# Performance work log

Hardware: AMD Instinct MI355X
Metric: run time of the kernel (lower is better)

The kernel has to match this reference:

```python
import jax, jax.numpy as jnp
import numpy as np

B, N, DIM, H, DH = 2, 2048, 1024, 16, 64
SOFTCAP = 50.0
SCALE = DH ** -0.5
EPS = 1e-12


def _rmsnorm(x, gamma):
    # F.normalize (l2norm over last dim) * sqrt(dim) * (gamma + 1)
    norm = jnp.maximum(jnp.linalg.norm(x, axis=-1, keepdims=True), EPS)
    return (x / norm) * (DIM ** 0.5) * (gamma + 1.0)


def _rotate_half(t):
    # interleaved pairs: (x1, x2) -> (-x2, x1), as in rotary_embedding_torch
    t = t.reshape(*t.shape[:-1], -1, 2)
    x1, x2 = t[..., 0], t[..., 1]
    return jnp.stack((-x2, x1), axis=-1).reshape(*t.shape[:-2], -1)


def _apply_rotary(freqs, t):
    # freqs: [n, d] broadcast over [b, h, n, d]
    return t * jnp.cos(freqs) + _rotate_half(t) * jnp.sin(freqs)


def setup_inputs() -> dict:
    key = jax.random.key(0)
    k0, k1, k2, k3, k4 = jax.random.split(key, 5)
    x = jax.random.normal(k0, (B, N, DIM), jnp.float32)
    gamma = jax.random.normal(k1, (DIM,), jnp.float32) * 0.02
    w_qkv = jax.random.normal(k2, (DIM, 3 * H * DH), jnp.float32) * 0.02
    w_out = jax.random.normal(k3, (H * DH, DIM), jnp.float32) * 0.02
    rotary_emb = jax.random.normal(k4, (N, DH), jnp.float32)
    attn_mask = jnp.broadcast_to(jnp.tril(jnp.ones((N, N), bool)), (B, N, N))
    return {"x": x, "attn_mask": attn_mask, "rotary_emb": rotary_emb,
            "gamma": gamma, "w_qkv": w_qkv, "w_out": w_out}


def reference(x, attn_mask, rotary_emb, gamma, w_qkv, w_out):
    x = _rmsnorm(x, gamma)
    qkv = (x @ w_qkv).reshape(B, N, 3, H, DH)        # b n (qkv h d)
    qkv = jnp.transpose(qkv, (2, 0, 3, 1, 4))        # qkv b h n d
    q, k, v = qkv[0], qkv[1], qkv[2]
    q = _apply_rotary(rotary_emb, q)
    k = _apply_rotary(rotary_emb, k)
    q = q * SCALE
    sim = jnp.einsum('bhid,bhjd->bhij', q, k)
    sim = jnp.tanh(sim / SOFTCAP) * SOFTCAP          # softclamp
    mask_value = -jnp.finfo(sim.dtype).max
    sim = jnp.where(attn_mask[:, None, :, :], sim, mask_value)
    attn = jax.nn.softmax(sim, axis=-1)
    out = jnp.einsum('bhij,bhjd->bhid', attn, v)
    out = jnp.transpose(out, (0, 2, 1, 3)).reshape(B, N, H * DH)  # b n (h d)
    return out @ w_out
```

## Files before the change

### kernel.cpp

```cpp
#include <hip/hip_runtime.h>
#include <hip/hip_bf16.h>

typedef unsigned short u16;
typedef unsigned int u32;
typedef __bf16 bf16x8 __attribute__((ext_vector_type(8)));
typedef float f32x4 __attribute__((ext_vector_type(4)));

#define NB 2
#define NSEQ 2048
#define NDIM 1024
#define NH 16
#define NDH 64

static __device__ __forceinline__ u16 f2bf(float f) {
  return __builtin_bit_cast(u16, (__bf16)f);
}
static __device__ __forceinline__ float bf2f(u16 u) {
  union { u32 u; float f; } a; a.u = ((u32)u) << 16; return a.f;
}
static __device__ __forceinline__ bf16x8 ldbf8(const u16* p) {
  return *(const bf16x8*)p;
}
static __device__ __forceinline__ f32x4 mfma16(bf16x8 a, bf16x8 b, f32x4 c) {
  return __builtin_amdgcn_mfma_f32_16x16x32_bf16(a, b, c, 0, 0, 0);
}
static __device__ __forceinline__ float fexp2(float x) {
  return __builtin_amdgcn_exp2f(x);
}
#define GLDS(g, d) __builtin_amdgcn_global_load_lds(                         \
    (const __attribute__((address_space(1))) void*)(g),                      \
    (__attribute__((address_space(3))) void*)(d), 16, 0, 0)

__global__ __launch_bounds__(256) void k_transpose(const float* __restrict__ in,
                                                   u16* __restrict__ out,
                                                   int R, int C) {
  __shared__ u16 tile[64][65];
  const int r0 = blockIdx.x * 64, c0 = blockIdx.y * 64;
  const int t = threadIdx.x;
  const int tr = t >> 6;
  const int tc = t & 63;
#pragma unroll 4
  for (int p = 0; p < 16; p++) {
    int r = p * 4 + tr;
    tile[r][tc] = f2bf(in[(size_t)(r0 + r) * C + (c0 + tc)]);
  }
  __syncthreads();
#pragma unroll 4
  for (int p = 0; p < 16; p++) {
    int rr = p * 4 + tr;
    out[(size_t)(c0 + rr) * R + (r0 + tc)] = tile[tc][rr];
  }
}

__global__ __launch_bounds__(256) void k_rmsnorm(const float* __restrict__ x,
                                                 const float* __restrict__ gamma,
                                                 u16* __restrict__ xn) {
  __shared__ float part[4];
  const int row = blockIdx.x;
  const int t = threadIdx.x;
  const float4 v = ((const float4*)(x + (size_t)row * NDIM))[t];
  float ss = v.x * v.x + v.y * v.y + v.z * v.z + v.w * v.w;
#pragma unroll
  for (int off = 1; off < 64; off <<= 1) ss += __shfl_xor(ss, off, 64);
  if ((t & 63) == 0) part[t >> 6] = ss;
  __syncthreads();
  const float tot = part[0] + part[1] + part[2] + part[3];
  const float scale = 32.0f / fmaxf(sqrtf(tot), 1e-12f);
  const float4 g = ((const float4*)gamma)[t];
  u16 o0 = f2bf(v.x * scale * (g.x + 1.0f));
  u16 o1 = f2bf(v.y * scale * (g.y + 1.0f));
  u16 o2 = f2bf(v.z * scale * (g.z + 1.0f));
  u16 o3 = f2bf(v.w * scale * (g.w + 1.0f));
  uint2 pv;
  pv.x = (u32)o0 | ((u32)o1 << 16);
  pv.y = (u32)o2 | ((u32)o3 << 16);
  *(uint2*)(xn + (size_t)row * NDIM + t * 4) = pv;
}

template <int EPI>
__global__ __launch_bounds__(256) void k_gemm_bt(const u16* __restrict__ A,
                                                 const u16* __restrict__ BT,
                                                 float* __restrict__ Of,
                                                 u16* __restrict__ O0,
                                                 u16* __restrict__ O1,
                                                 u16* __restrict__ O2) {
  constexpr int KD = 1024, BK = 64, NT = KD / BK;
  __shared__ u16 As[128 * BK];
  __shared__ u16 Bs[128 * BK];
  const int m0 = blockIdx.x * 128, n0 = blockIdx.y * 128;
  const int t = threadIdx.x;
  const int w = t >> 6, l = t & 63, lo = l & 15, hi = l >> 4;
  const int wr = (w >> 1) * 64, wc = (w & 1) * 64;
  const int srow = w * 32 + (l >> 3);
  const int sch  = (l & 7) ^ (l >> 3);
  const u16* ag = A  + (size_t)(m0 + srow) * KD + sch * 8;
  const u16* bg = BT + (size_t)(n0 + srow) * KD + sch * 8;
  u16* asd = As + w * 2048;
  u16* bsd = Bs + w * 2048;
  f32x4 acc[4][4] = {};
  for (int kt = 0; kt < NT; kt++) {
    const int k0 = kt * BK;
    __syncthreads();
#pragma unroll
    for (int i = 0; i < 4; i++) {
      GLDS(ag + k0 + i * 8 * KD, asd + i * 512);
      GLDS(bg + k0 + i * 8 * KD, bsd + i * 512);
    }
    __syncthreads();
    bf16x8 af[4][2], bb[4][2];
#pragma unroll
    for (int i = 0; i < 4; i++) {
      const int Ra = wr + i * 16 + lo, xa = Ra & 7;
      af[i][0] = ldbf8(&As[Ra * 64 + ((hi ^ xa) << 3)]);
      af[i][1] = ldbf8(&As[Ra * 64 + (((4 + hi) ^ xa) << 3)]);
      const int Rb = wc + i * 16 + lo, xb = Rb & 7;
      bb[i][0] = ldbf8(&Bs[Rb * 64 + ((hi ^ xb) << 3)]);
      bb[i][1] = ldbf8(&Bs[Rb * 64 + (((4 + hi) ^ xb) << 3)]);
    }
#pragma unroll
    for (int i = 0; i < 4; i++)
#pragma unroll
      for (int j = 0; j < 4; j++) {
        acc[i][j] = mfma16(af[i][0], bb[j][0], acc[i][j]);
        acc[i][j] = mfma16(af[i][1], bb[j][1], acc[i][j]);
      }
  }
#pragma unroll
  for (int i = 0; i < 4; i++) {
#pragma unroll
    for (int j = 0; j < 4; j++) {
      const int gr0 = m0 + wr + i * 16 + hi * 4;
      const int gc = n0 + wc + j * 16 + lo;
#pragma unroll
      for (int r = 0; r < 4; r++) {
        const int row = gr0 + r;
        if (EPI == 0) {
          Of[(size_t)row * 1024 + gc] = acc[i][j][r];
        } else {
          const u16 bv = f2bf(acc[i][j][r]);
          const int which = gc >> 10, rem = gc & 1023;
          const int h = rem >> 6, dh = rem & 63;
          const int b = row >> 11, ns = row & 2047;
          if (which == 2) {
            O2[(((size_t)b * NH + h) * NDH + dh) * NSEQ + ns] = bv;
          } else {
            const size_t idx = ((((size_t)b * NH + h) * NSEQ) + ns) * NDH + dh;
            (which == 0 ? O0 : O1)[idx] = bv;
          }
        }
      }
    }
  }
}

__global__ __launch_bounds__(256) void k_rotary(u16* __restrict__ qb,
                                                u16* __restrict__ kb,
                                                const float* __restrict__ rot) {
  const int gi = blockIdx.x * 256 + threadIdx.x;
  const int half = gi >> 19;
  const int i = gi & ((1 << 19) - 1);
  u16* buf = half ? kb : qb;
  const float scale = half ? 1.0f : 0.125f;
  const int d0 = (i & 7) * 8;
  const int n = (i >> 3) & (NSEQ - 1);
  union { uint4 v; u16 s[8]; } u;
  u.v = *(const uint4*)(buf + (size_t)i * 8);
  float fr[8];
  *(float4*)&fr[0] = *(const float4*)(rot + n * NDH + d0);
  *(float4*)&fr[4] = *(const float4*)(rot + n * NDH + d0 + 4);
  union { uint4 v; u16 s[8]; } o;
#pragma unroll
  for (int p = 0; p < 4; p++) {
    float a = bf2f(u.s[2 * p]), b = bf2f(u.s[2 * p + 1]);
    float s0, c0, s1, c1;
    __sincosf(fr[2 * p], &s0, &c0);
    __sincosf(fr[2 * p + 1], &s1, &c1);
    o.s[2 * p] = f2bf((a * c0 - b * s0) * scale);
    o.s[2 * p + 1] = f2bf((b * c1 + a * s1) * scale);
  }
  *(uint4*)(buf + (size_t)i * 8) = o.v;
}

#define KCH(row, ch) ((((ch) ^ ((row) & 7)) * 8))
__global__ __launch_bounds__(128) void k_attn(const u16* __restrict__ Q,
                                              const u16* __restrict__ K,
                                              const u16* __restrict__ Vt,
                                              u16* __restrict__ O) {
  __shared__ u16 Ks[2][4096];
  __shared__ u16 Vs[2][4096];
  __shared__ u16 Ps[2][16][64];
  const int pr = blockIdx.x >> 5;
  const int bh = blockIdx.x & 31;
  const int b = bh >> 4, h = bh & 15;
  const size_t base = (size_t)bh * (NSEQ * NDH);
  const int t = threadIdx.x;
  const int w = t >> 6, l = t & 63, lo = l & 15, hi = l >> 4;

  const int rl = l >> 3;
  const int sc8 = ((l & 7) ^ rl) * 8;
  const size_t vtb = (size_t)bh * NDH * NSEQ;

#define STAGE(bb, kt_)                                                        \
  {                                                                           \
    _Pragma("unroll")                                                         \
    for (int i_ = 0; i_ < 4; i_++) {                                          \
      const int R_ = (w * 4 + i_) * 8 + rl;                                   \
      GLDS(K + base + (size_t)((kt_) * 64 + R_) * NDH + sc8,                  \
           &Ks[bb][(w * 4 + i_) * 512]);                                      \
      GLDS(Vt + vtb + (size_t)R_ * NSEQ + (kt_) * 64 + sc8,                   \
           &Vs[bb][(w * 4 + i_) * 512]);                                      \
    }                                                                         \
  }

  int cur = 0;
  STAGE(0, 0);

#pragma unroll
  for (int half = 0; half < 2; half++) {
    const int qt = half ? (63 - pr) : pr;
    const int q0 = qt * 32;
    bf16x8 aq0, aq1;
    {
      const u16* qp = Q + base + (size_t)(q0 + w * 16 + lo) * NDH;
      aq0 = ldbf8(qp + hi * 8);
      aq1 = ldbf8(qp + 32 + hi * 8);
    }
    f32x4 accO[4] = {};
    float l_part[4] = {0.f, 0.f, 0.f, 0.f};
    const int nkt = (qt >> 1) + 1;
    const int ktd = qt >> 1;
    const int rowg = q0 + w * 16 + hi * 4;

    for (int kt = 0; kt < nkt; kt++) {
      __syncthreads();
      if (kt + 1 < nkt) {
        STAGE(cur ^ 1, kt + 1);
      } else if (half == 0) {
        STAGE(cur ^ 1, 0);
      }

      const u16* ks = Ks[cur];
      const u16* vs = Vs[cur];
      f32x4 s[4];
#pragma unroll
      for (int nt = 0; nt < 4; nt++) {
        const int kr = nt * 16 + lo;
        f32x4 z = {};
        z = mfma16(aq0, ldbf8(&ks[kr * 64 + KCH(kr, hi)]), z);
        z = mfma16(aq1, ldbf8(&ks[kr * 64 + KCH(kr, 4 + hi)]), z);
        s[nt] = z;
      }
      const bool diag = (kt == ktd);
#pragma unroll
      for (int nt = 0; nt < 4; nt++) {
        const int col = kt * 64 + nt * 16 + lo;
#pragma unroll
        for (int r = 0; r < 4; r++) {
          const float v = s[nt][r];
          const float u = v * v;
          const float poly = fmaf(u, fmaf(u, 2.1333333e-8f, -1.3333333e-4f), 1.0f);
          float p = fexp2(v * 1.44269504f * poly);
          if (diag && col > rowg + r) p = 0.0f;
          s[nt][r] = p;
          l_part[r] += p;
        }
      }
#pragma unroll
      for (int nt = 0; nt < 4; nt++)
#pragma unroll
        for (int r = 0; r < 4; r++) {
          const int row = hi * 4 + r;
          Ps[w][row][KCH(row, 2 * nt + (lo >> 3)) + (lo & 7)] = f2bf(s[nt][r]);
        }

      const bf16x8 ap0 = ldbf8(&Ps[w][lo][KCH(lo, hi)]);
      const bf16x8 ap1 = ldbf8(&Ps[w][lo][KCH(lo, 4 + hi)]);
#pragma unroll
      for (int dt = 0; dt < 4; dt++) {
        const int d = dt * 16 + lo;
        accO[dt] = mfma16(ap0, ldbf8(&vs[d * 64 + KCH(d, hi)]), accO[dt]);
        accO[dt] = mfma16(ap1, ldbf8(&vs[d * 64 + KCH(d, 4 + hi)]), accO[dt]);
      }
      cur ^= 1;
    }
    float lr[4];
#pragma unroll
    for (int r = 0; r < 4; r++) {
      float lv = l_part[r];
      lv += __shfl_xor(lv, 1, 64);
      lv += __shfl_xor(lv, 2, 64);
      lv += __shfl_xor(lv, 4, 64);
      lv += __shfl_xor(lv, 8, 64);
      lr[r] = __builtin_amdgcn_rcpf(lv);
    }
#pragma unroll
    for (int dt = 0; dt < 4; dt++) {
#pragma unroll
      for (int r = 0; r < 4; r++) {
        const int row = rowg + r;
        const float v = accO[dt][r] * lr[r];
        const size_t idx = (((size_t)(b * NSEQ + row)) * NH + h) * NDH + dt * 16 + lo;
        O[idx] = f2bf(v);
      }
    }
  }
#undef STAGE
}

extern "C" void kernel_launch(void* const* d_in, const int* in_sizes, int n_in,
                              void* d_out, int out_size, void* d_ws, size_t ws_size,
                              hipStream_t stream) {
  const float* x     = (const float*)d_in[0];
  const float* rot   = (const float*)d_in[2];
  const float* gamma = (const float*)d_in[3];
  const float* wqkv  = (const float*)d_in[4];
  const float* wout  = (const float*)d_in[5];

  char* ws = (char*)d_ws;
  u16* xn    = (u16*)(ws);
  u16* wqkvT = (u16*)(ws + (size_t)( 8u << 20));
  u16* woutT = (u16*)(ws + (size_t)(14u << 20));
  u16* qb    = (u16*)(ws + (size_t)(16u << 20));
  u16* kb    = (u16*)(ws + (size_t)(24u << 20));
  u16* vt    = (u16*)(ws + (size_t)(32u << 20));
  u16* ob    = xn;

  k_transpose<<<dim3(16, 48), 256, 0, stream>>>(wqkv, wqkvT, 1024, 3072);
  k_transpose<<<dim3(16, 16), 256, 0, stream>>>(wout, woutT, 1024, 1024);
  k_rmsnorm<<<4096, 256, 0, stream>>>(x, gamma, xn);
  k_gemm_bt<1><<<dim3(32, 24), 256, 0, stream>>>(xn, wqkvT, nullptr, qb, kb, vt);
  k_rotary<<<4096, 256, 0, stream>>>(qb, kb, rot);
  k_attn<<<1024, 128, 0, stream>>>(qb, kb, vt, ob);
  k_gemm_bt<0><<<dim3(32, 8), 256, 0, stream>>>(ob, woutT, (float*)d_out, nullptr, nullptr, nullptr);
}
```

Before: 131.7 us.

## Process paired causal query tiles together over shared K/V stream; precompute rotary table

The attention kernel now walks the K/V tiles once for both the low and high query tiles of a block pair. It runs the low tile only while its causal range lasts, so each staged K/V tile is reused by two query tiles instead of being reloaded in a second pass. Separately, sin/cos of the rotary angles are computed once per (position, pair) into a table in workspace, so the rotary kernel no longer recomputes them for both q and k across batches and heads. This costs extra registers for two accumulator sets, a second P scratch slot in shared memory, and one small extra kernel launch.

```diff
diff --git a/kernel.cpp b/kernel.cpp
--- a/kernel.cpp
+++ b/kernel.cpp
@@ -153,30 +153,36 @@
   }
 }
 
+__global__ __launch_bounds__(256) void k_rotprep(const float* __restrict__ rot,
+                                                 float4* __restrict__ tab) {
+  const int i = blockIdx.x * 256 + threadIdx.x;
+  const int n = i >> 5, p = i & 31;
+  const float fe = rot[n * NDH + 2 * p], fo = rot[n * NDH + 2 * p + 1];
+  float ce, se, co, so;
+  __sincosf(fe, &se, &ce);
+  __sincosf(fo, &so, &co);
+  tab[i] = make_float4(ce, se, co, so);
+}
+
 __global__ __launch_bounds__(256) void k_rotary(u16* __restrict__ qb,
                                                 u16* __restrict__ kb,
-                                                const float* __restrict__ rot) {
+                                                const float4* __restrict__ tab) {
   const int gi = blockIdx.x * 256 + threadIdx.x;
   const int half = gi >> 19;
   const int i = gi & ((1 << 19) - 1);
   u16* buf = half ? kb : qb;
   const float scale = half ? 1.0f : 0.125f;
-  const int d0 = (i & 7) * 8;
+  const int p0 = (i & 7) * 4;
   const int n = (i >> 3) & (NSEQ - 1);
   union { uint4 v; u16 s[8]; } u;
   u.v = *(const uint4*)(buf + (size_t)i * 8);
-  float fr[8];
-  *(float4*)&fr[0] = *(const float4*)(rot + n * NDH + d0);
-  *(float4*)&fr[4] = *(const float4*)(rot + n * NDH + d0 + 4);
   union { uint4 v; u16 s[8]; } o;
 #pragma unroll
-  for (int p = 0; p < 4; p++) {
-    float a = bf2f(u.s[2 * p]), b = bf2f(u.s[2 * p + 1]);
-    float s0, c0, s1, c1;
-    __sincosf(fr[2 * p], &s0, &c0);
-    __sincosf(fr[2 * p + 1], &s1, &c1);
-    o.s[2 * p] = f2bf((a * c0 - b * s0) * scale);
-    o.s[2 * p + 1] = f2bf((b * c1 + a * s1) * scale);
+  for (int pp = 0; pp < 4; pp++) {
+    const float4 tb = tab[n * 32 + p0 + pp];
+    const float a = bf2f(u.s[2 * pp]), b = bf2f(u.s[2 * pp + 1]);
+    o.s[2 * pp]     = f2bf((a * tb.x - b * tb.y) * scale);
+    o.s[2 * pp + 1] = f2bf((b * tb.z + a * tb.w) * scale);
   }
   *(uint4*)(buf + (size_t)i * 8) = o.v;
 }
@@ -188,13 +194,13 @@
                                               u16* __restrict__ O) {
   __shared__ u16 Ks[2][4096];
   __shared__ u16 Vs[2][4096];
-  __shared__ u16 Ps[2][16][64];
+  __shared__ u16 Ps[2][2][16][64];
   const int pr = blockIdx.x >> 5;
   const int bh = blockIdx.x & 31;
   const int b = bh >> 4, h = bh & 15;
   const size_t base = (size_t)bh * (NSEQ * NDH);
   const int t = threadIdx.x;
-  const int w = t >> 6, l = t & 63, lo = l & 15, hi = l >> 4;
+  const int w = t >> 6, l = t & 63, lq = l & 15, hf = l >> 4;
 
   const int rl = l >> 3;
   const int sc8 = ((l & 7) ^ rl) * 8;
@@ -212,98 +218,110 @@
     }                                                                         \
   }
 
+  const int qtL = pr, qtH = 63 - pr;
+  const int nktL = (qtL >> 1) + 1, nktH = (qtH >> 1) + 1;
+  const int q0L = qtL * 32, q0H = qtH * 32;
+  const int rowgL = q0L + w * 16 + hf * 4;
+  const int rowgH = q0H + w * 16 + hf * 4;
+
+  bf16x8 aqL0, aqL1, aqH0, aqH1;
+  {
+    const u16* qp = Q + base + (size_t)(q0L + w * 16 + lq) * NDH;
+    aqL0 = ldbf8(qp + hf * 8);
+    aqL1 = ldbf8(qp + 32 + hf * 8);
+    const u16* qh = Q + base + (size_t)(q0H + w * 16 + lq) * NDH;
+    aqH0 = ldbf8(qh + hf * 8);
+    aqH1 = ldbf8(qh + 32 + hf * 8);
+  }
+  f32x4 accL[4] = {}, accH[4] = {};
+  float lpL[4] = {0.f, 0.f, 0.f, 0.f}, lpH[4] = {0.f, 0.f, 0.f, 0.f};
+
   int cur = 0;
   STAGE(0, 0);
 
-#pragma unroll
-  for (int half = 0; half < 2; half++) {
-    const int qt = half ? (63 - pr) : pr;
-    const int q0 = qt * 32;
-    bf16x8 aq0, aq1;
-    {
-      const u16* qp = Q + base + (size_t)(q0 + w * 16 + lo) * NDH;
-      aq0 = ldbf8(qp + hi * 8);
-      aq1 = ldbf8(qp + 32 + hi * 8);
+  for (int kt = 0; kt < nktH; kt++) {
+    __syncthreads();
+    if (kt + 1 < nktH) STAGE(cur ^ 1, kt + 1);
+    const u16* ks = Ks[cur];
+    const u16* vs = Vs[cur];
+
+#define QTILE(AQ0, AQ1, ACC, LP, ROWG, PSLOT, DIAG)                           \
+    {                                                                         \
+      f32x4 s[4];                                                             \
+      _Pragma("unroll")                                                       \
+      for (int nt = 0; nt < 4; nt++) {                                        \
+        const int kr = nt * 16 + lq;                                          \
+        f32x4 z = {};                                                         \
+        z = mfma16(AQ0, ldbf8(&ks[kr * 64 + KCH(kr, hf)]), z);                \
+        z = mfma16(AQ1, ldbf8(&ks[kr * 64 + KCH(kr, 4 + hf)]), z);            \
+        s[nt] = z;                                                            \
+      }                                                                       \
+      _Pragma("unroll")                                                       \
+      for (int nt = 0; nt < 4; nt++) {                                        \
+        const int col = kt * 64 + nt * 16 + lq;                               \
+        _Pragma("unroll")                                                     \
+        for (int r = 0; r < 4; r++) {                                         \
+          const float v = s[nt][r];                                           \
+          const float uu = v * v;                                             \
+          const float poly =                                                  \
+              fmaf(uu, fmaf(uu, 2.1333333e-8f, -1.3333333e-4f), 1.0f);        \
+          float p = fexp2(v * 1.44269504f * poly);                            \
+          if ((DIAG) && col > (ROWG) + r) p = 0.0f;                           \
+          s[nt][r] = p;                                                       \
+          LP[r] += p;                                                         \
+        }                                                                     \
+      }                                                                       \
+      _Pragma("unroll")                                                       \
+      for (int nt = 0; nt < 4; nt++)                                          \
+        _Pragma("unroll")                                                     \
+        for (int r = 0; r < 4; r++) {                                         \
+          const int row = hf * 4 + r;                                         \
+          Ps[w][PSLOT][row][KCH(row, 2 * nt + (lq >> 3)) + (lq & 7)] =        \
+              f2bf(s[nt][r]);                                                 \
+        }                                                                     \
+      const bf16x8 ap0 = ldbf8(&Ps[w][PSLOT][lq][KCH(lq, hf)]);               \
+      const bf16x8 ap1 = ldbf8(&Ps[w][PSLOT][lq][KCH(lq, 4 + hf)]);           \
+      _Pragma("unroll")                                                       \
+      for (int dt = 0; dt < 4; dt++) {                                        \
+        const int d = dt * 16 + lq;                                           \
+        ACC[dt] = mfma16(ap0, ldbf8(&vs[d * 64 + KCH(d, hf)]), ACC[dt]);      \
+        ACC[dt] = mfma16(ap1, ldbf8(&vs[d * 64 + KCH(d, 4 + hf)]), ACC[dt]);  \
+      }                                                                       \
     }
-    f32x4 accO[4] = {};
-    float l_part[4] = {0.f, 0.f, 0.f, 0.f};
-    const int nkt = (qt >> 1) + 1;
-    const int ktd = qt >> 1;
-    const int rowg = q0 + w * 16 + hi * 4;
-
-    for (int kt = 0; kt < nkt; kt++) {
-      __syncthreads();
-      if (kt + 1 < nkt) {
-        STAGE(cur ^ 1, kt + 1);
-      } else if (half == 0) {
-        STAGE(cur ^ 1, 0);
-      }
-
-      const u16* ks = Ks[cur];
-      const u16* vs = Vs[cur];
-      f32x4 s[4];
-#pragma unroll
-      for (int nt = 0; nt < 4; nt++) {
-        const int kr = nt * 16 + lo;
-        f32x4 z = {};
-        z = mfma16(aq0, ldbf8(&ks[kr * 64 + KCH(kr, hi)]), z);
-        z = mfma16(aq1, ldbf8(&ks[kr * 64 + KCH(kr, 4 + hi)]), z);
-        s[nt] = z;
-      }
-      const bool diag = (kt == ktd);
-#pragma unroll
-      for (int nt = 0; nt < 4; nt++) {
-        const int col = kt * 64 + nt * 16 + lo;
-#pragma unroll
-        for (int r = 0; r < 4; r++) {
-          const float v = s[nt][r];
-          const float u = v * v;
-          const float poly = fmaf(u, fmaf(u, 2.1333333e-8f, -1.3333333e-4f), 1.0f);
-          float p = fexp2(v * 1.44269504f * poly);
-          if (diag && col > rowg + r) p = 0.0f;
-          s[nt][r] = p;
-          l_part[r] += p;
-        }
-      }
-#pragma unroll
-      for (int nt = 0; nt < 4; nt++)
-#pragma unroll
-        for (int r = 0; r < 4; r++) {
-          const int row = hi * 4 + r;
-          Ps[w][row][KCH(row, 2 * nt + (lo >> 3)) + (lo & 7)] = f2bf(s[nt][r]);
-        }
-
-      const bf16x8 ap0 = ldbf8(&Ps[w][lo][KCH(lo, hi)]);
-      const bf16x8 ap1 = ldbf8(&Ps[w][lo][KCH(lo, 4 + hi)]);
-#pragma unroll
-      for (int dt = 0; dt < 4; dt++) {
-        const int d = dt * 16 + lo;
-        accO[dt] = mfma16(ap0, ldbf8(&vs[d * 64 + KCH(d, hi)]), accO[dt]);
-        accO[dt] = mfma16(ap1, ldbf8(&vs[d * 64 + KCH(d, 4 + hi)]), accO[dt]);
-      }
-      cur ^= 1;
-    }
-    float lr[4];
-#pragma unroll
-    for (int r = 0; r < 4; r++) {
-      float lv = l_part[r];
-      lv += __shfl_xor(lv, 1, 64);
-      lv += __shfl_xor(lv, 2, 64);
-      lv += __shfl_xor(lv, 4, 64);
-      lv += __shfl_xor(lv, 8, 64);
-      lr[r] = __builtin_amdgcn_rcpf(lv);
-    }
-#pragma unroll
-    for (int dt = 0; dt < 4; dt++) {
-#pragma unroll
-      for (int r = 0; r < 4; r++) {
-        const int row = rowg + r;
-        const float v = accO[dt][r] * lr[r];
-        const size_t idx = (((size_t)(b * NSEQ + row)) * NH + h) * NDH + dt * 16 + lo;
-        O[idx] = f2bf(v);
-      }
-    }
-  }
+
+    if (kt < nktL) QTILE(aqL0, aqL1, accL, lpL, rowgL, 0, kt == nktL - 1);
+    QTILE(aqH0, aqH1, accH, lpH, rowgH, 1, kt == nktH - 1);
+#undef QTILE
+    cur ^= 1;
+  }
+
+#define EPI(ACC, LP, ROWG)                                                    \
+  {                                                                           \
+    float lr[4];                                                              \
+    _Pragma("unroll")                                                         \
+    for (int r = 0; r < 4; r++) {                                             \
+      float lv = LP[r];                                                       \
+      lv += __shfl_xor(lv, 1, 64);                                            \
+      lv += __shfl_xor(lv, 2, 64);                                            \
+      lv += __shfl_xor(lv, 4, 64);                                            \
+      lv += __shfl_xor(lv, 8, 64);                                            \
+      lr[r] = __builtin_amdgcn_rcpf(lv);                                      \
+    }                                                                         \
+    _Pragma("unroll")                                                         \
+    for (int dt = 0; dt < 4; dt++) {                                          \
+      _Pragma("unroll")                                                       \
+      for (int r = 0; r < 4; r++) {                                           \
+        const int row = (ROWG) + r;                                           \
+        const float v = ACC[dt][r] * lr[r];                                   \
+        const size_t idx =                                                    \
+            (((size_t)(b * NSEQ + row)) * NH + h) * NDH + dt * 16 + lq;       \
+        O[idx] = f2bf(v);                                                     \
+      }                                                                       \
+    }                                                                         \
+  }
+  EPI(accL, lpL, rowgL);
+  EPI(accH, lpH, rowgH);
+#undef EPI
 #undef STAGE
 }
 
@@ -323,13 +341,15 @@
   u16* qb    = (u16*)(ws + (size_t)(16u << 20));
   u16* kb    = (u16*)(ws + (size_t)(24u << 20));
   u16* vt    = (u16*)(ws + (size_t)(32u << 20));
+  float4* rtab = (float4*)(ws);
   u16* ob    = xn;
 
   k_transpose<<<dim3(16, 48), 256, 0, stream>>>(wqkv, wqkvT, 1024, 3072);
   k_transpose<<<dim3(16, 16), 256, 0, stream>>>(wout, woutT, 1024, 1024);
   k_rmsnorm<<<4096, 256, 0, stream>>>(x, gamma, xn);
   k_gemm_bt<1><<<dim3(32, 24), 256, 0, stream>>>(xn, wqkvT, nullptr, qb, kb, vt);
-  k_rotary<<<4096, 256, 0, stream>>>(qb, kb, rot);
+  k_rotprep<<<256, 256, 0, stream>>>(rot, rtab);
+  k_rotary<<<4096, 256, 0, stream>>>(qb, kb, rtab);
   k_attn<<<1024, 128, 0, stream>>>(qb, kb, vt, ob);
   k_gemm_bt<0><<<dim3(32, 8), 256, 0, stream>>>(ob, woutT, (float*)d_out, nullptr, nullptr, nullptr);
 }
```

Result: no change. 133.5 us (+1.4%).

## Split attention into 32-key tiles with one query tile per block; precompute rotary table

Applied to the files above, without the earlier changes.

The attention kernel no longer pairs two query tiles per block. It now launches one block per 32-row query tile, heaviest tiles first, with 32-key K/V tiles, half-size LDS buffers and a new XOR swizzle for the V tile. This gives twice as many blocks and smaller shared memory per block, which is meant to raise occupancy and shorten the tail. The cost is the pairing's load balance and a shorter MFMA chain per iteration. Separately, rotary sin/cos values are computed once per (n, pair) into a table, so the rotary kernel no longer repeats them for q and k, at the cost of an extra small kernel launch.

```diff
diff --git a/kernel.cpp b/kernel.cpp
--- a/kernel.cpp
+++ b/kernel.cpp
@@ -153,30 +153,36 @@
   }
 }
 
+__global__ __launch_bounds__(256) void k_rotprep(const float* __restrict__ rot,
+                                                 float4* __restrict__ tab) {
+  const int i = blockIdx.x * 256 + threadIdx.x;
+  const int n = i >> 5, p = i & 31;
+  const float fe = rot[n * NDH + 2 * p], fo = rot[n * NDH + 2 * p + 1];
+  float ce, se, co, so;
+  __sincosf(fe, &se, &ce);
+  __sincosf(fo, &so, &co);
+  tab[i] = make_float4(ce, se, co, so);
+}
+
 __global__ __launch_bounds__(256) void k_rotary(u16* __restrict__ qb,
                                                 u16* __restrict__ kb,
-                                                const float* __restrict__ rot) {
+                                                const float4* __restrict__ tab) {
   const int gi = blockIdx.x * 256 + threadIdx.x;
   const int half = gi >> 19;
   const int i = gi & ((1 << 19) - 1);
   u16* buf = half ? kb : qb;
   const float scale = half ? 1.0f : 0.125f;
-  const int d0 = (i & 7) * 8;
+  const int p0 = (i & 7) * 4;
   const int n = (i >> 3) & (NSEQ - 1);
   union { uint4 v; u16 s[8]; } u;
   u.v = *(const uint4*)(buf + (size_t)i * 8);
-  float fr[8];
-  *(float4*)&fr[0] = *(const float4*)(rot + n * NDH + d0);
-  *(float4*)&fr[4] = *(const float4*)(rot + n * NDH + d0 + 4);
   union { uint4 v; u16 s[8]; } o;
 #pragma unroll
-  for (int p = 0; p < 4; p++) {
-    float a = bf2f(u.s[2 * p]), b = bf2f(u.s[2 * p + 1]);
-    float s0, c0, s1, c1;
-    __sincosf(fr[2 * p], &s0, &c0);
-    __sincosf(fr[2 * p + 1], &s1, &c1);
-    o.s[2 * p] = f2bf((a * c0 - b * s0) * scale);
-    o.s[2 * p + 1] = f2bf((b * c1 + a * s1) * scale);
+  for (int pp = 0; pp < 4; pp++) {
+    const float4 tb = tab[n * 32 + p0 + pp];
+    const float a = bf2f(u.s[2 * pp]), b = bf2f(u.s[2 * pp + 1]);
+    o.s[2 * pp]     = f2bf((a * tb.x - b * tb.y) * scale);
+    o.s[2 * pp + 1] = f2bf((b * tb.z + a * tb.w) * scale);
   }
   *(uint4*)(buf + (size_t)i * 8) = o.v;
 }
@@ -186,122 +192,111 @@
                                               const u16* __restrict__ K,
                                               const u16* __restrict__ Vt,
                                               u16* __restrict__ O) {
-  __shared__ u16 Ks[2][4096];
-  __shared__ u16 Vs[2][4096];
-  __shared__ u16 Ps[2][16][64];
-  const int pr = blockIdx.x >> 5;
+  __shared__ u16 Ks[2][2048];
+  __shared__ u16 Vs[2][2048];
+  __shared__ u16 Ps[2][16][40];
+  const int qt = 63 - (blockIdx.x >> 5);
   const int bh = blockIdx.x & 31;
   const int b = bh >> 4, h = bh & 15;
   const size_t base = (size_t)bh * (NSEQ * NDH);
   const int t = threadIdx.x;
-  const int w = t >> 6, l = t & 63, lo = l & 15, hi = l >> 4;
-
+  const int w = t >> 6, l = t & 63, lq = l & 15, hf = l >> 4;
   const int rl = l >> 3;
   const int sc8 = ((l & 7) ^ rl) * 8;
-  const size_t vtb = (size_t)bh * NDH * NSEQ;
+  const int vr = l >> 2;
+  const int q0 = qt * 32;
+  const int nkt = qt + 1;
+  const int rowg = q0 + w * 16 + hf * 4;
+
+  bf16x8 aq0, aq1;
+  {
+    const u16* qp = Q + base + (size_t)(q0 + w * 16 + lq) * NDH;
+    aq0 = ldbf8(qp + hf * 8);
+    aq1 = ldbf8(qp + 32 + hf * 8);
+  }
+  f32x4 accO[4] = {};
+  float lp[4] = {0.f, 0.f, 0.f, 0.f};
 
 #define STAGE(bb, kt_)                                                        \
   {                                                                           \
     _Pragma("unroll")                                                         \
-    for (int i_ = 0; i_ < 4; i_++) {                                          \
-      const int R_ = (w * 4 + i_) * 8 + rl;                                   \
-      GLDS(K + base + (size_t)((kt_) * 64 + R_) * NDH + sc8,                  \
-           &Ks[bb][(w * 4 + i_) * 512]);                                      \
-      GLDS(Vt + vtb + (size_t)R_ * NSEQ + (kt_) * 64 + sc8,                   \
-           &Vs[bb][(w * 4 + i_) * 512]);                                      \
+    for (int i_ = 0; i_ < 2; i_++) {                                          \
+      const int ii = w * 2 + i_;                                              \
+      GLDS(K + base + (size_t)((kt_) * 32 + ii * 8 + rl) * NDH + sc8,         \
+           &Ks[bb][ii * 512]);                                                \
+      const int dR = ii * 16 + vr;                                            \
+      const int vc = (((l & 3) ^ (dR & 3) ^ ((dR >> 2) & 3))) * 8;            \
+      GLDS(Vt + base + (size_t)dR * NSEQ + (kt_) * 32 + vc,                   \
+           &Vs[bb][ii * 512]);                                                \
     }                                                                         \
   }
 
   int cur = 0;
   STAGE(0, 0);
 
-#pragma unroll
-  for (int half = 0; half < 2; half++) {
-    const int qt = half ? (63 - pr) : pr;
-    const int q0 = qt * 32;
-    bf16x8 aq0, aq1;
-    {
-      const u16* qp = Q + base + (size_t)(q0 + w * 16 + lo) * NDH;
-      aq0 = ldbf8(qp + hi * 8);
-      aq1 = ldbf8(qp + 32 + hi * 8);
-    }
-    f32x4 accO[4] = {};
-    float l_part[4] = {0.f, 0.f, 0.f, 0.f};
-    const int nkt = (qt >> 1) + 1;
-    const int ktd = qt >> 1;
-    const int rowg = q0 + w * 16 + hi * 4;
-
-    for (int kt = 0; kt < nkt; kt++) {
-      __syncthreads();
-      if (kt + 1 < nkt) {
-        STAGE(cur ^ 1, kt + 1);
-      } else if (half == 0) {
-        STAGE(cur ^ 1, 0);
+  for (int kt = 0; kt < nkt; kt++) {
+    __syncthreads();
+    if (kt + 1 < nkt) STAGE(cur ^ 1, kt + 1);
+    const u16* ks = Ks[cur];
+    const u16* vs = Vs[cur];
+
+    f32x4 s[2];
+#pragma unroll
+    for (int nt = 0; nt < 2; nt++) {
+      const int kr = nt * 16 + lq;
+      f32x4 z = {};
+      z = mfma16(aq0, ldbf8(&ks[kr * 64 + KCH(kr, hf)]), z);
+      z = mfma16(aq1, ldbf8(&ks[kr * 64 + KCH(kr, 4 + hf)]), z);
+      s[nt] = z;
+    }
+    const bool diag = (kt == qt);
+#pragma unroll
+    for (int nt = 0; nt < 2; nt++) {
+      const int col = kt * 32 + nt * 16 + lq;
+#pragma unroll
+      for (int r = 0; r < 4; r++) {
+        const float v = s[nt][r];
+        const float uu = v * v;
+        const float poly = fmaf(uu, fmaf(uu, 2.1333333e-8f, -1.3333333e-4f), 1.0f);
+        float p = fexp2(v * 1.44269504f * poly);
+        if (diag && col > rowg + r) p = 0.0f;
+        s[nt][r] = p;
+        lp[r] += p;
       }
-
-      const u16* ks = Ks[cur];
-      const u16* vs = Vs[cur];
-      f32x4 s[4];
-#pragma unroll
-      for (int nt = 0; nt < 4; nt++) {
-        const int kr = nt * 16 + lo;
-        f32x4 z = {};
-        z = mfma16(aq0, ldbf8(&ks[kr * 64 + KCH(kr, hi)]), z);
-        z = mfma16(aq1, ldbf8(&ks[kr * 64 + KCH(kr, 4 + hi)]), z);
-        s[nt] = z;
-      }
-      const bool diag = (kt == ktd);
-#pragma unroll
-      for (int nt = 0; nt < 4; nt++) {
-        const int col = kt * 64 + nt * 16 + lo;
-#pragma unroll
-        for (int r = 0; r < 4; r++) {
-          const float v = s[nt][r];
-          const float u = v * v;
-          const float poly = fmaf(u, fmaf(u, 2.1333333e-8f, -1.3333333e-4f), 1.0f);
-          float p = fexp2(v * 1.44269504f * poly);
-          if (diag && col > rowg + r) p = 0.0f;
-          s[nt][r] = p;
-          l_part[r] += p;
-        }
-      }
-#pragma unroll
-      for (int nt = 0; nt < 4; nt++)
-#pragma unroll
-        for (int r = 0; r < 4; r++) {
-          const int row = hi * 4 + r;
-          Ps[w][row][KCH(row, 2 * nt + (lo >> 3)) + (lo & 7)] = f2bf(s[nt][r]);
-        }
-
-      const bf16x8 ap0 = ldbf8(&Ps[w][lo][KCH(lo, hi)]);
-      const bf16x8 ap1 = ldbf8(&Ps[w][lo][KCH(lo, 4 + hi)]);
-#pragma unroll
-      for (int dt = 0; dt < 4; dt++) {
-        const int d = dt * 16 + lo;
-        accO[dt] = mfma16(ap0, ldbf8(&vs[d * 64 + KCH(d, hi)]), accO[dt]);
-        accO[dt] = mfma16(ap1, ldbf8(&vs[d * 64 + KCH(d, 4 + hi)]), accO[dt]);
-      }
-      cur ^= 1;
-    }
-    float lr[4];
+    }
+#pragma unroll
+    for (int nt = 0; nt < 2; nt++)
+#pragma unroll
+      for (int r = 0; r < 4; r++)
+        Ps[w][hf * 4 + r][nt * 16 + lq] = f2bf(s[nt][r]);
+
+    const bf16x8 ap0 = ldbf8(&Ps[w][lq][hf * 8]);
+    const int vph = (hf ^ (lq & 3) ^ ((lq >> 2) & 3)) * 8;
+#pragma unroll
+    for (int dt = 0; dt < 4; dt++) {
+      const int d = dt * 16 + lq;
+      accO[dt] = mfma16(ap0, ldbf8(&vs[d * 32 + vph]), accO[dt]);
+    }
+    cur ^= 1;
+  }
+  float lr[4];
+#pragma unroll
+  for (int r = 0; r < 4; r++) {
+    float lv = lp[r];
+    lv += __shfl_xor(lv, 1, 64);
+    lv += __shfl_xor(lv, 2, 64);
+    lv += __shfl_xor(lv, 4, 64);
+    lv += __shfl_xor(lv, 8, 64);
+    lr[r] = __builtin_amdgcn_rcpf(lv);
+  }
+#pragma unroll
+  for (int dt = 0; dt < 4; dt++) {
 #pragma unroll
     for (int r = 0; r < 4; r++) {
-      float lv = l_part[r];
-      lv += __shfl_xor(lv, 1, 64);
-      lv += __shfl_xor(lv, 2, 64);
-      lv += __shfl_xor(lv, 4, 64);
-      lv += __shfl_xor(lv, 8, 64);
-      lr[r] = __builtin_amdgcn_rcpf(lv);
-    }
-#pragma unroll
-    for (int dt = 0; dt < 4; dt++) {
-#pragma unroll
-      for (int r = 0; r < 4; r++) {
-        const int row = rowg + r;
-        const float v = accO[dt][r] * lr[r];
-        const size_t idx = (((size_t)(b * NSEQ + row)) * NH + h) * NDH + dt * 16 + lo;
-        O[idx] = f2bf(v);
-      }
+      const int row = rowg + r;
+      const float v = accO[dt][r] * lr[r];
+      const size_t idx = (((size_t)(b * NSEQ + row)) * NH + h) * NDH + dt * 16 + lq;
+      O[idx] = f2bf(v);
     }
   }
 #undef STAGE
@@ -323,13 +318,15 @@
   u16* qb    = (u16*)(ws + (size_t)(16u << 20));
   u16* kb    = (u16*)(ws + (size_t)(24u << 20));
   u16* vt    = (u16*)(ws + (size_t)(32u << 20));
+  float4* rtab = (float4*)(ws);
   u16* ob    = xn;
 
   k_transpose<<<dim3(16, 48), 256, 0, stream>>>(wqkv, wqkvT, 1024, 3072);
   k_transpose<<<dim3(16, 16), 256, 0, stream>>>(wout, woutT, 1024, 1024);
   k_rmsnorm<<<4096, 256, 0, stream>>>(x, gamma, xn);
   k_gemm_bt<1><<<dim3(32, 24), 256, 0, stream>>>(xn, wqkvT, nullptr, qb, kb, vt);
-  k_rotary<<<4096, 256, 0, stream>>>(qb, kb, rot);
-  k_attn<<<1024, 128, 0, stream>>>(qb, kb, vt, ob);
+  k_rotprep<<<256, 256, 0, stream>>>(rot, rtab);
+  k_rotary<<<4096, 256, 0, stream>>>(qb, kb, rtab);
+  k_attn<<<2048, 128, 0, stream>>>(qb, kb, vt, ob);
   k_gemm_bt<0><<<dim3(32, 8), 256, 0, stream>>>(ob, woutT, (float*)d_out, nullptr, nullptr, nullptr);
 }
```

Measured after the change: 143.4 us. 1.09x slower.

## Double-buffer GEMM LDS tiles with BK=32 and use 64-row M tiles

Applied to the files above, without the earlier changes.

The bf16 GEMM kernel now double-buffers its shared-memory tiles, issuing the global-to-LDS loads for the next K slice before computing the current one. This removes one barrier per iteration and overlaps load latency with MFMA work. K slices shrink to 32 and the M tile is a template parameter, set to 64 for both GEMMs, which doubles the grid size to fill more CUs. The cost is lower per-block reuse (more B-tile reloads) and a new LDS swizzle pattern.

```diff
diff --git a/kernel.cpp b/kernel.cpp
--- a/kernel.cpp
+++ b/kernel.cpp
@@ -77,56 +77,77 @@
   *(uint2*)(xn + (size_t)row * NDIM + t * 4) = pv;
 }
 
-template <int EPI>
+template <int EPI, int BM>
 __global__ __launch_bounds__(256) void k_gemm_bt(const u16* __restrict__ A,
                                                  const u16* __restrict__ BT,
                                                  float* __restrict__ Of,
                                                  u16* __restrict__ O0,
                                                  u16* __restrict__ O1,
                                                  u16* __restrict__ O2) {
-  constexpr int KD = 1024, BK = 64, NT = KD / BK;
-  __shared__ u16 As[128 * BK];
-  __shared__ u16 Bs[128 * BK];
-  const int m0 = blockIdx.x * 128, n0 = blockIdx.y * 128;
+  constexpr int KD = 1024, BK = 32, NT = KD / BK;
+  constexpr int MI = BM / 32;
+  constexpr int ANI = BM / 64;
+  __shared__ u16 As[2][BM * BK];
+  __shared__ u16 Bs[2][128 * BK];
+  const int m0 = blockIdx.x * BM, n0 = blockIdx.y * 128;
   const int t = threadIdx.x;
   const int w = t >> 6, l = t & 63, lo = l & 15, hi = l >> 4;
-  const int wr = (w >> 1) * 64, wc = (w & 1) * 64;
-  const int srow = w * 32 + (l >> 3);
-  const int sch  = (l & 7) ^ (l >> 3);
-  const u16* ag = A  + (size_t)(m0 + srow) * KD + sch * 8;
-  const u16* bg = BT + (size_t)(n0 + srow) * KD + sch * 8;
-  u16* asd = As + w * 2048;
-  u16* bsd = Bs + w * 2048;
-  f32x4 acc[4][4] = {};
+  const int wr = (w >> 1) * (BM / 2), wc = (w & 1) * 64;
+  const int schunk = ((l & 3) ^ ((l >> 2) & 3) ^ (l >> 4)) * 8;
+  const u16* agp[ANI > 0 ? ANI : 1];
+  const u16* bgp[2];
+  u16* asd[ANI > 0 ? ANI : 1];
+  u16* bsd[2];
+#pragma unroll
+  for (int i = 0; i < ANI; i++) {
+    const int rA = (w * ANI + i) * 16 + (l >> 2);
+    agp[i] = A + (size_t)(m0 + rA) * KD + schunk;
+    asd[i] = (u16*)As + (w * ANI + i) * 512;
+  }
+#pragma unroll
+  for (int i = 0; i < 2; i++) {
+    const int rB = (w * 2 + i) * 16 + (l >> 2);
+    bgp[i] = BT + (size_t)(n0 + rB) * KD + schunk;
+    bsd[i] = (u16*)Bs + (w * 2 + i) * 512;
+  }
+  const int sx = (lo & 3) ^ ((lo >> 2) & 3);
+  f32x4 acc[MI][4] = {};
+
+#define GSTAGE(bb, kt_)                                                       \
+  {                                                                           \
+    _Pragma("unroll")                                                         \
+    for (int i_ = 0; i_ < ANI; i_++)                                          \
+      GLDS(agp[i_] + (kt_) * BK, asd[i_] + (bb) * BM * BK);                   \
+    _Pragma("unroll")                                                         \
+    for (int i_ = 0; i_ < 2; i_++)                                            \
+      GLDS(bgp[i_] + (kt_) * BK, bsd[i_] + (bb) * 128 * BK);                  \
+  }
+
+  int cur = 0;
+  GSTAGE(0, 0);
   for (int kt = 0; kt < NT; kt++) {
-    const int k0 = kt * BK;
     __syncthreads();
-#pragma unroll
-    for (int i = 0; i < 4; i++) {
-      GLDS(ag + k0 + i * 8 * KD, asd + i * 512);
-      GLDS(bg + k0 + i * 8 * KD, bsd + i * 512);
-    }
-    __syncthreads();
-    bf16x8 af[4][2], bb[4][2];
-#pragma unroll
-    for (int i = 0; i < 4; i++) {
-      const int Ra = wr + i * 16 + lo, xa = Ra & 7;
-      af[i][0] = ldbf8(&As[Ra * 64 + ((hi ^ xa) << 3)]);
-      af[i][1] = ldbf8(&As[Ra * 64 + (((4 + hi) ^ xa) << 3)]);
-      const int Rb = wc + i * 16 + lo, xb = Rb & 7;
-      bb[i][0] = ldbf8(&Bs[Rb * 64 + ((hi ^ xb) << 3)]);
-      bb[i][1] = ldbf8(&Bs[Rb * 64 + (((4 + hi) ^ xb) << 3)]);
-    }
-#pragma unroll
-    for (int i = 0; i < 4; i++)
-#pragma unroll
-      for (int j = 0; j < 4; j++) {
-        acc[i][j] = mfma16(af[i][0], bb[j][0], acc[i][j]);
-        acc[i][j] = mfma16(af[i][1], bb[j][1], acc[i][j]);
-      }
-  }
-#pragma unroll
-  for (int i = 0; i < 4; i++) {
+    if (kt + 1 < NT) GSTAGE(cur ^ 1, kt + 1);
+    const u16* as = (const u16*)As + cur * BM * BK;
+    const u16* bs = (const u16*)Bs + cur * 128 * BK;
+    bf16x8 af[MI], bb[4];
+#pragma unroll
+    for (int i = 0; i < MI; i++)
+      af[i] = ldbf8(&as[(wr + i * 16 + lo) * BK + ((hi ^ sx) << 3)]);
+#pragma unroll
+    for (int j = 0; j < 4; j++)
+      bb[j] = ldbf8(&bs[(wc + j * 16 + lo) * BK + ((hi ^ sx) << 3)]);
+#pragma unroll
+    for (int i = 0; i < MI; i++)
+#pragma unroll
+      for (int j = 0; j < 4; j++)
+        acc[i][j] = mfma16(af[i], bb[j], acc[i][j]);
+    cur ^= 1;
+  }
+#undef GSTAGE
+
+#pragma unroll
+  for (int i = 0; i < MI; i++) {
 #pragma unroll
     for (int j = 0; j < 4; j++) {
       const int gr0 = m0 + wr + i * 16 + hi * 4;
@@ -328,8 +349,8 @@
   k_transpose<<<dim3(16, 48), 256, 0, stream>>>(wqkv, wqkvT, 1024, 3072);
   k_transpose<<<dim3(16, 16), 256, 0, stream>>>(wout, woutT, 1024, 1024);
   k_rmsnorm<<<4096, 256, 0, stream>>>(x, gamma, xn);
-  k_gemm_bt<1><<<dim3(32, 24), 256, 0, stream>>>(xn, wqkvT, nullptr, qb, kb, vt);
+  k_gemm_bt<1, 64><<<dim3(64, 24), 256, 0, stream>>>(xn, wqkvT, nullptr, qb, kb, vt);
   k_rotary<<<4096, 256, 0, stream>>>(qb, kb, rot);
   k_attn<<<1024, 128, 0, stream>>>(qb, kb, vt, ob);
-  k_gemm_bt<0><<<dim3(32, 8), 256, 0, stream>>>(ob, woutT, (float*)d_out, nullptr, nullptr, nullptr);
-}
+  k_gemm_bt<0, 64><<<dim3(64, 8), 256, 0, stream>>>(ob, woutT, (float*)d_out, nullptr, nullptr, nullptr);
+}
```

Result: slower. 156.0 us (+18.5%).
